# Kernel tuning notes

Hardware: AMD Instinct MI355X
Metric: run time of the kernel (lower is better)

Reference implementation:

```python
import jax, jax.numpy as jnp
import numpy as np
from jax import lax

B, S, H = 32, 512, 128
NEG_INF = -1e30  # matches util.masked_softmax's large negative fill


def setup_inputs() -> dict:
    key = jax.random.key(0)
    ks = jax.random.split(key, 10)
    sc = 0.05
    vp = jax.random.normal(ks[0], (B, S, 2 * H), dtype=jnp.float32)
    # valid lengths in [S//2, S]; packed loop runs max(lengths) steps
    p_s_lengths = jax.random.randint(ks[1], (B,), S // 2, S + 1, dtype=jnp.int32)
    W_vP  = jax.random.normal(ks[2], (H, 2 * H), dtype=jnp.float32) * sc      # linear_vP.weight
    W_vPt = jax.random.normal(ks[3], (H, 2 * H), dtype=jnp.float32) * sc      # linear_vPt.weight
    w_vT  = jax.random.normal(ks[4], (H,), dtype=jnp.float32) * sc            # linear_vT.weight (1,H) -> vector
    W_g   = jax.random.normal(ks[5], (4 * H, 4 * H), dtype=jnp.float32) * sc  # g.weight
    W_ih  = jax.random.normal(ks[6], (3 * H, 4 * H), dtype=jnp.float32) * sc  # GRUCell.weight_ih
    W_hh  = jax.random.normal(ks[7], (3 * H, H), dtype=jnp.float32) * sc      # GRUCell.weight_hh
    b_ih  = jax.random.normal(ks[8], (3 * H,), dtype=jnp.float32) * sc
    b_hh  = jax.random.normal(ks[9], (3 * H,), dtype=jnp.float32) * sc
    return dict(vp=vp, p_s_lengths=p_s_lengths, W_vP=W_vP, W_vPt=W_vPt,
                w_vT=w_vT, W_g=W_g, W_ih=W_ih, W_hh=W_hh, b_ih=b_ih, b_hh=b_hh)


def _self_attn_rnn(vp, p_s_lengths, W_vP, W_vPt, w_vT, W_g, W_ih, W_hh, b_ih, b_hh):
    Bb, Ss, H2 = vp.shape
    Hh = H2 // 2
    s_idx = jnp.arange(Ss)

    # reverse_enc: reverse each sequence only over its valid prefix
    rev_idx = jnp.where(s_idx[None, :] < p_s_lengths[:, None],
                        p_s_lengths[:, None] - 1 - s_idx[None, :], s_idx[None, :])
    rev_vp = jnp.take_along_axis(vp, rev_idx[:, :, None], axis=1)

    bidir_vp = jnp.concatenate([vp, rev_vp], axis=0)       # (2B,S,2H) inputs per step
    vp2 = jnp.concatenate([vp, vp], axis=0)                 # (2B,S,2H) attention memory (forward order!)
    len2 = jnp.concatenate([p_s_lengths, p_s_lengths], 0)   # (2B,)

    keyp = jnp.einsum('bsd,hd->bsh', vp2, W_vP)             # precompute linear_vP(vp)
    seq_mask = s_idx[None, :] < len2[:, None]               # (2B,S)

    def step(h, inputs):
        x_t, active = inputs                                # (2B,2H), (2B,)
        q = x_t @ W_vPt.T                                   # (2B,H)
        logits = jnp.tanh(keyp + q[:, None, :]) @ w_vT      # (2B,S)
        a = jax.nn.softmax(jnp.where(seq_mask, logits, NEG_INF), axis=1)
        ct = jnp.einsum('bs,bsd->bd', a, vp2)               # (2B,2H)
        vpc = jnp.concatenate([x_t, ct], axis=-1)           # (2B,4H)
        gt = jax.nn.sigmoid(vpc @ W_g.T)
        xin = gt * vpc
        gi = xin @ W_ih.T + b_ih
        gh = h @ W_hh.T + b_hh
        ir, iz, inn = jnp.split(gi, 3, axis=-1)
        hr, hz, hn = jnp.split(gh, 3, axis=-1)
        r = jax.nn.sigmoid(ir + hr)
        z = jax.nn.sigmoid(iz + hz)
        n = jnp.tanh(inn + r * hn)
        h_new = (1.0 - z) * n + z * h
        # packed semantics: inactive (padded) slots keep zeros and never update again
        h_new = jnp.where(active[:, None], h_new, 0.0)
        return h_new, h_new

    xs = (jnp.swapaxes(bidir_vp, 0, 1), seq_mask.T)          # (S,2B,2H), (S,2B)
    h0 = jnp.zeros((2 * Bb, Hh), dtype=vp.dtype)
    _, hs = lax.scan(jax.checkpoint(step), h0, xs)           # hs: (S,2B,H)
    hp = jnp.swapaxes(hs, 0, 1)                              # (2B,S,H)
    # original concatenates fwd half and rev half on feature dim (rev half stays in reversed time order)
    return jnp.concatenate([hp[:Bb], hp[Bb:]], axis=-1)      # (B,S,2H)


def reference(vp, p_s_lengths, W_vP, W_vPt, w_vT, W_g, W_ih, W_hh, b_ih, b_hh):
    # dropout is identity at inference (training=False)
    return _self_attn_rnn(vp, p_s_lengths, W_vP, W_vPt, w_vT, W_g, W_ih, W_hh, b_ih, b_hh)
```

## Files before the change

kernel.cpp:

```cpp
#include <hip/hip_runtime.h>
#include <hip/hip_fp16.h>

#define BB 32
#define SS 512
#define HH 128
#define D2 256
#define D3 384
#define D4 512

#define OFF_TK  0
#define OFF_TQ  (OFF_TK + BB*SS*HH)
#define OFF_CT  (OFF_TQ + BB*SS*HH)
#define OFF_GI  (OFF_CT + BB*SS*D2)
#define OFF_F16 (OFF_GI + BB*SS*D3)
#define F16_WG  0
#define F16_WIH (F16_WG + D4*D4)
#define F16_W2  (F16_WIH + D3*D4)

typedef _Float16 f16x8 __attribute__((ext_vector_type(8)));
typedef _Float16 f16x4 __attribute__((ext_vector_type(4)));
typedef float    f32x4 __attribute__((ext_vector_type(4)));
typedef _Float16 h2_t  __attribute__((ext_vector_type(2)));

__device__ __forceinline__ float fast_tanh(float x) {
  float ax = fabsf(x);
  float e  = __expf(-2.0f * ax);
  float t  = __fdividef(1.0f - e, 1.0f + e);
  return x < 0.0f ? -t : t;
}
__device__ __forceinline__ float sigm(float x) {
  return __fdividef(1.0f, 1.0f + __expf(-x));
}

__global__ __launch_bounds__(256) void k0_prep(
    const float* __restrict__ Wg, const float* __restrict__ Wih,
    const float* __restrict__ Wvp, const float* __restrict__ Wvpt,
    float* __restrict__ ws) {
  int i = blockIdx.x * 256 + threadIdx.x;
  _Float16* f16b = (_Float16*)(ws + OFF_F16);
  if (i < D4 * D4) {
    f16b[F16_WG + i] = (_Float16)Wg[i];
  } else if (i < D4 * D4 + D3 * D4) {
    int j = i - D4 * D4;
    f16b[F16_WIH + j] = (_Float16)Wih[j];
  } else {
    int j = i - D4 * D4 - D3 * D4;
    f16b[F16_W2 + j] = (_Float16)(j < HH * D2 ? Wvp[j] : Wvpt[j - HH * D2]);
  }
}

__global__ __launch_bounds__(256, 2) void k1_keyq(const float* __restrict__ vp,
                                                  float* __restrict__ ws) {
  __shared__ __align__(16) _Float16 vpH[64 * 256];
  int tid = threadIdx.x;
  int rows0 = blockIdx.x * 64;

  #pragma unroll
  for (int i = 0; i < 8; ++i) {
    int u = tid + i * 256;
    int r = u >> 5, c8 = u & 31;
    const float* src = vp + (size_t)(rows0 + r) * D2 + c8 * 8;
    float4 a = *(const float4*)src;
    float4 b = *(const float4*)(src + 4);
    f16x8 h;
    h[0]=(_Float16)a.x; h[1]=(_Float16)a.y; h[2]=(_Float16)a.z; h[3]=(_Float16)a.w;
    h[4]=(_Float16)b.x; h[5]=(_Float16)b.y; h[6]=(_Float16)b.z; h[7]=(_Float16)b.w;
    *(f16x8*)(&vpH[r * 256 + (c8 ^ (r & 7)) * 8]) = h;
  }
  __syncthreads();

  const _Float16* W2 = (const _Float16*)(ws + OFF_F16) + F16_W2;
  int w = tid >> 6, l = tid & 63;
  int lr = l & 15, lk = (l >> 4) * 8;

  f32x4 acc[4][4];
  #pragma unroll
  for (int m = 0; m < 4; ++m)
    #pragma unroll
    for (int n = 0; n < 4; ++n) acc[m][n] = (f32x4){0.f, 0.f, 0.f, 0.f};

  for (int kc = 0; kc < 8; ++kc) {
    int k = kc * 32 + lk;
    f16x8 bf[4];
    #pragma unroll
    for (int n = 0; n < 4; ++n) {
      int r = n * 16 + lr;
      bf[n] = *(const f16x8*)(&vpH[r * 256 + (((k >> 3) ^ (r & 7))) * 8]);
    }
    #pragma unroll
    for (int m = 0; m < 4; ++m) {
      int c = w * 64 + m * 16 + lr;
      f16x8 af = *(const f16x8*)(W2 + (size_t)c * 256 + k);
      #pragma unroll
      for (int n = 0; n < 4; ++n)
        acc[m][n] = __builtin_amdgcn_mfma_f32_16x16x32_f16(af, bf[n], acc[m][n], 0, 0, 0);
    }
  }

  int b = rows0 >> 9;
  int s0 = rows0 & 511;
  float* ekT = ws + OFF_TK + (size_t)b * HH * SS;
  float* eqp = ws + OFF_TQ + (size_t)b * SS * HH;
  #pragma unroll
  for (int m = 0; m < 4; ++m) {
    int c0 = w * 64 + m * 16 + (l >> 4) * 4;
    #pragma unroll
    for (int n = 0; n < 4; ++n) {
      int s = s0 + n * 16 + lr;
      float v[4];
      #pragma unroll
      for (int j = 0; j < 4; ++j) {
        float z = fminf(fmaxf(2.0f * acc[m][n][j], -60.0f), 60.0f);
        v[j] = __expf(z);
      }
      if (c0 < HH) {
        #pragma unroll
        for (int j = 0; j < 4; ++j)
          ekT[(size_t)(c0 + j) * SS + s] = v[j];
      } else {
        float4 o; o.x = v[0]; o.y = v[1]; o.z = v[2]; o.w = v[3];
        *(float4*)(eqp + (size_t)s * HH + (c0 - HH)) = o;
      }
    }
  }
}

__global__ __launch_bounds__(256) void k2_attn(const float* __restrict__ vp,
                                               const int* __restrict__ lens,
                                               const float* __restrict__ wvt,
                                               float* __restrict__ ws) {
  int bid = blockIdx.x;
  int b  = (bid & 7) * 4 + ((bid >> 3) & 3);
  int t0 = (bid >> 5) * 16;
  int len = lens[b];
  if (t0 >= len) return;
  int nt = min(16, len - t0);

  __shared__ float L[16][SS];
  __shared__ float Eqs[16][HH];
  __shared__ float inv_sum[16];

  int tid = threadIdx.x;
  const float* EkT = ws + OFF_TK + (size_t)b * HH * SS;
  const float* Eq  = ws + OFF_TQ + (size_t)b * SS * HH;

  for (int idx = tid; idx < 16 * HH; idx += 256) {
    int i = idx >> 7, h = idx & 127;
    Eqs[i][h] = Eq[(size_t)(t0 + i) * HH + h];
  }
  __syncthreads();

  for (int sc = 0; sc < 2; ++sc) {
    int s = tid + sc * 256;
    if (s < len) {
      float acc[16] = {};
      for (int h4 = 0; h4 < 32; ++h4) {
        float k0 = EkT[(size_t)(h4 * 4 + 0) * SS + s];
        float k1 = EkT[(size_t)(h4 * 4 + 1) * SS + s];
        float k2v = EkT[(size_t)(h4 * 4 + 2) * SS + s];
        float k3 = EkT[(size_t)(h4 * 4 + 3) * SS + s];
        const float4 w4 = *(const float4*)(wvt + h4 * 4);
        #pragma unroll
        for (int t = 0; t < 16; ++t) {
          const float4 q4 = *(const float4*)(&Eqs[t][h4 * 4]);
          float r0 = __builtin_amdgcn_rcpf(fmaf(k0, q4.x, 1.0f));
          float r1 = __builtin_amdgcn_rcpf(fmaf(k1, q4.y, 1.0f));
          float r2 = __builtin_amdgcn_rcpf(fmaf(k2v, q4.z, 1.0f));
          float r3 = __builtin_amdgcn_rcpf(fmaf(k3, q4.w, 1.0f));
          float a = acc[t];
          a = fmaf(w4.x, r0, a);
          a = fmaf(w4.y, r1, a);
          a = fmaf(w4.z, r2, a);
          a = fmaf(w4.w, r3, a);
          acc[t] = a;
        }
      }
      #pragma unroll
      for (int t = 0; t < 16; ++t) L[t][s] = -2.0f * acc[t];
    }
  }
  __syncthreads();

  {
    int w = tid >> 6, lane = tid & 63;
    for (int ii = 0; ii < 4; ++ii) {
      int i = w + ii * 4;
      if (i < nt) {
        float m = -1e30f;
        for (int s = lane; s < len; s += 64) m = fmaxf(m, L[i][s]);
        #pragma unroll
        for (int off = 32; off > 0; off >>= 1) m = fmaxf(m, __shfl_xor(m, off));
        float sm = 0.0f;
        for (int s = lane; s < len; s += 64) {
          float e = __expf(L[i][s] - m);
          L[i][s] = e;
          sm += e;
        }
        #pragma unroll
        for (int off = 32; off > 0; off >>= 1) sm += __shfl_xor(sm, off);
        if (lane == 0) inv_sum[i] = __fdividef(1.0f, sm);
      }
    }
  }
  __syncthreads();

  int d4 = (tid & 63) * 4;
  int tg = tid >> 6;
  float4 acc4[4] = {};
  const float* vpb = vp + (size_t)b * SS * D2;
  int s = 0;
  for (; s + 4 <= len; s += 4) {
    #pragma unroll
    for (int u = 0; u < 4; ++u) {
      float4 v4 = *(const float4*)(vpb + (size_t)(s + u) * D2 + d4);
      #pragma unroll
      for (int j = 0; j < 4; ++j) {
        float p = L[tg * 4 + j][s + u];
        acc4[j].x = fmaf(p, v4.x, acc4[j].x);
        acc4[j].y = fmaf(p, v4.y, acc4[j].y);
        acc4[j].z = fmaf(p, v4.z, acc4[j].z);
        acc4[j].w = fmaf(p, v4.w, acc4[j].w);
      }
    }
  }
  for (; s < len; ++s) {
    float4 v4 = *(const float4*)(vpb + (size_t)s * D2 + d4);
    #pragma unroll
    for (int j = 0; j < 4; ++j) {
      float p = L[tg * 4 + j][s];
      acc4[j].x = fmaf(p, v4.x, acc4[j].x);
      acc4[j].y = fmaf(p, v4.y, acc4[j].y);
      acc4[j].z = fmaf(p, v4.z, acc4[j].z);
      acc4[j].w = fmaf(p, v4.w, acc4[j].w);
    }
  }
  float* ctg = ws + OFF_CT + ((size_t)b * SS + t0) * D2;
  #pragma unroll
  for (int j = 0; j < 4; ++j) {
    int t = tg * 4 + j;
    if (t < nt) {
      float is = inv_sum[t];
      float4 o;
      o.x = acc4[j].x * is; o.y = acc4[j].y * is;
      o.z = acc4[j].z * is; o.w = acc4[j].w * is;
      *(float4*)(ctg + (size_t)t * D2 + d4) = o;
    }
  }
}

__global__ __launch_bounds__(256, 2) void k3_gates(const float* __restrict__ vp,
                                                   const int* __restrict__ lens,
                                                   const float* __restrict__ bih,
                                                   float* __restrict__ ws) {
  int b = blockIdx.y;
  int len = lens[b];
  int t0 = blockIdx.x * 32;
  if (t0 >= len) return;

  __shared__ __align__(16) _Float16 vpcH[32 * 512];
  int tid = threadIdx.x;
  const float* ct = ws + OFF_CT;

  #pragma unroll
  for (int i = 0; i < 8; ++i) {
    int u = tid + i * 256;
    int r = u >> 6, c8 = u & 63;
    int c = c8 * 8;
    const float* src = (c < D2) ? (vp + ((size_t)b * SS + t0 + r) * D2 + c)
                                : (ct + ((size_t)b * SS + t0 + r) * D2 + (c - D2));
    float4 a = *(const float4*)src;
    float4 bb = *(const float4*)(src + 4);
    f16x8 h;
    h[0]=(_Float16)a.x;  h[1]=(_Float16)a.y;  h[2]=(_Float16)a.z;  h[3]=(_Float16)a.w;
    h[4]=(_Float16)bb.x; h[5]=(_Float16)bb.y; h[6]=(_Float16)bb.z; h[7]=(_Float16)bb.w;
    *(f16x8*)(&vpcH[r * 512 + (c8 ^ (r & 7)) * 8]) = h;
  }
  __syncthreads();

  const _Float16* WgH  = (const _Float16*)(ws + OFF_F16) + F16_WG;
  const _Float16* WihH = (const _Float16*)(ws + OFF_F16) + F16_WIH;
  int w = tid >> 6, l = tid & 63;
  int lr = l & 15, lk = (l >> 4) * 8;

  f32x4 acc[8][2];
  #pragma unroll
  for (int m = 0; m < 8; ++m) { acc[m][0] = (f32x4){0.f,0.f,0.f,0.f}; acc[m][1] = (f32x4){0.f,0.f,0.f,0.f}; }

  for (int kc = 0; kc < 16; ++kc) {
    int k = kc * 32 + lk;
    f16x8 bf[2];
    #pragma unroll
    for (int n = 0; n < 2; ++n) {
      int r = n * 16 + lr;
      bf[n] = *(const f16x8*)(&vpcH[r * 512 + (((k >> 3) ^ (r & 7))) * 8]);
    }
    #pragma unroll
    for (int m = 0; m < 8; ++m) {
      int c = w * 128 + m * 16 + lr;
      f16x8 af = *(const f16x8*)(WgH + (size_t)c * 512 + k);
      acc[m][0] = __builtin_amdgcn_mfma_f32_16x16x32_f16(af, bf[0], acc[m][0], 0, 0, 0);
      acc[m][1] = __builtin_amdgcn_mfma_f32_16x16x32_f16(af, bf[1], acc[m][1], 0, 0, 0);
    }
  }

  f16x4 xq[8][2];
  #pragma unroll
  for (int m = 0; m < 8; ++m) {
    int c0 = w * 128 + m * 16 + (l >> 4) * 4;
    #pragma unroll
    for (int n = 0; n < 2; ++n) {
      int r = n * 16 + lr;
      int ea = r * 512 + (((c0 >> 3) ^ (r & 7))) * 8 + (c0 & 7);
      f16x4 vq = *(const f16x4*)(&vpcH[ea]);
      f16x4 xo;
      #pragma unroll
      for (int j = 0; j < 4; ++j)
        xo[j] = (_Float16)(sigm(acc[m][n][j]) * (float)vq[j]);
      xq[m][n] = xo;
    }
  }
  __syncthreads();
  #pragma unroll
  for (int m = 0; m < 8; ++m) {
    int c0 = w * 128 + m * 16 + (l >> 4) * 4;
    #pragma unroll
    for (int n = 0; n < 2; ++n) {
      int r = n * 16 + lr;
      int ea = r * 512 + (((c0 >> 3) ^ (r & 7))) * 8 + (c0 & 7);
      *(f16x4*)(&vpcH[ea]) = xq[m][n];
    }
  }
  __syncthreads();

  f32x4 gacc[6][2];
  #pragma unroll
  for (int m = 0; m < 6; ++m) { gacc[m][0] = (f32x4){0.f,0.f,0.f,0.f}; gacc[m][1] = (f32x4){0.f,0.f,0.f,0.f}; }

  for (int kc = 0; kc < 16; ++kc) {
    int k = kc * 32 + lk;
    f16x8 bf[2];
    #pragma unroll
    for (int n = 0; n < 2; ++n) {
      int r = n * 16 + lr;
      bf[n] = *(const f16x8*)(&vpcH[r * 512 + (((k >> 3) ^ (r & 7))) * 8]);
    }
    #pragma unroll
    for (int m = 0; m < 6; ++m) {
      int c = w * 96 + m * 16 + lr;
      f16x8 af = *(const f16x8*)(WihH + (size_t)c * 512 + k);
      gacc[m][0] = __builtin_amdgcn_mfma_f32_16x16x32_f16(af, bf[0], gacc[m][0], 0, 0, 0);
      gacc[m][1] = __builtin_amdgcn_mfma_f32_16x16x32_f16(af, bf[1], gacc[m][1], 0, 0, 0);
    }
  }

  float* gig = ws + OFF_GI;
  #pragma unroll
  for (int m = 0; m < 6; ++m) {
    int c0 = w * 96 + m * 16 + (l >> 4) * 4;
    float4 bq = *(const float4*)(bih + c0);
    #pragma unroll
    for (int n = 0; n < 2; ++n) {
      int r = n * 16 + lr;
      float4 o;
      o.x = gacc[m][n][0] + bq.x;
      o.y = gacc[m][n][1] + bq.y;
      o.z = gacc[m][n][2] + bq.z;
      o.w = gacc[m][n][3] + bq.w;
      *(float4*)(gig + ((size_t)b * SS + t0 + r) * D3 + c0) = o;
    }
  }
}

__global__ __launch_bounds__(128, 1) void k4_scan(const float* __restrict__ whh,
                                                  const float* __restrict__ bhh,
                                                  const int* __restrict__ lens,
                                                  const float* __restrict__ ws,
                                                  float* __restrict__ out) {
  int bid = blockIdx.x;
  int xcd = bid & 7, dir = (bid >> 3) & 1, q = bid >> 4;
  int b = xcd * 4 + q;
  int len = lens[b];
  int tid = threadIdx.x;
  const float* gi = ws + OFF_GI + (size_t)b * SS * D3;

  h2_t w0[64], w1[64], w2[64];
  {
    const float* r0 = whh + (size_t)tid * HH;
    const float* r1 = whh + (size_t)(tid + 128) * HH;
    const float* r2 = whh + (size_t)(tid + 256) * HH;
    #pragma unroll
    for (int k = 0; k < 64; ++k) {
      w0[k] = h2_t{(_Float16)r0[2 * k], (_Float16)r0[2 * k + 1]};
      w1[k] = h2_t{(_Float16)r1[2 * k], (_Float16)r1[2 * k + 1]};
      w2[k] = h2_t{(_Float16)r2[2 * k], (_Float16)r2[2 * k + 1]};
    }
  }
  float bh0 = bhh[tid], bh1 = bhh[tid + 128], bh2 = bhh[tid + 256];

  __shared__ __align__(16) _Float16 hbuf[2][128];
  hbuf[0][tid] = (_Float16)0.0f;
  float h_own = 0.0f;

  float* outb = out + (size_t)b * SS * D2 + dir * HH;

#define K4_BAR() do {                                                          \
    asm volatile("s_waitcnt lgkmcnt(0)" ::: "memory");                         \
    __builtin_amdgcn_s_barrier();                                              \
    __builtin_amdgcn_sched_barrier(0);                                         \
  } while (0)

#define K4_PF(gx0, gx1, gx2, tnext) do {                                       \
    int tp = (tnext) < len ? (tnext) : (len - 1);                              \
    int tgp = dir ? (len - 1 - tp) : tp;                                       \
    const float* gp = gi + (size_t)tgp * D3;                                   \
    gx0 = gp[tid]; gx1 = gp[tid + 128]; gx2 = gp[tid + 256];                   \
  } while (0)

#define K4_STEP(gx0, gx1, gx2, tstep, PB) do {                                 \
    const f16x8* hb8 = (const f16x8*)hbuf[PB];                                 \
    float a00 = 0.f, a01 = 0.f, a02 = 0.f, a03 = 0.f;                          \
    float a10 = 0.f, a11 = 0.f, a12 = 0.f, a13 = 0.f;                          \
    float a20 = 0.f, a21 = 0.f, a22 = 0.f, a23 = 0.f;                          \
    _Pragma("unroll")                                                          \
    for (int k8 = 0; k8 < 16; ++k8) {                                          \
      f16x8 hv = hb8[k8];                                                      \
      h2_t p0 = __builtin_shufflevector(hv, hv, 0, 1);                         \
      h2_t p1 = __builtin_shufflevector(hv, hv, 2, 3);                         \
      h2_t p2 = __builtin_shufflevector(hv, hv, 4, 5);                         \
      h2_t p3 = __builtin_shufflevector(hv, hv, 6, 7);                         \
      a00 = __builtin_amdgcn_fdot2(p0, w0[4 * k8 + 0], a00, false);            \
      a01 = __builtin_amdgcn_fdot2(p1, w0[4 * k8 + 1], a01, false);            \
      a02 = __builtin_amdgcn_fdot2(p2, w0[4 * k8 + 2], a02, false);            \
      a03 = __builtin_amdgcn_fdot2(p3, w0[4 * k8 + 3], a03, false);            \
      a10 = __builtin_amdgcn_fdot2(p0, w1[4 * k8 + 0], a10, false);            \
      a11 = __builtin_amdgcn_fdot2(p1, w1[4 * k8 + 1], a11, false);            \
      a12 = __builtin_amdgcn_fdot2(p2, w1[4 * k8 + 2], a12, false);            \
      a13 = __builtin_amdgcn_fdot2(p3, w1[4 * k8 + 3], a13, false);            \
      a20 = __builtin_amdgcn_fdot2(p0, w2[4 * k8 + 0], a20, false);            \
      a21 = __builtin_amdgcn_fdot2(p1, w2[4 * k8 + 1], a21, false);            \
      a22 = __builtin_amdgcn_fdot2(p2, w2[4 * k8 + 2], a22, false);            \
      a23 = __builtin_amdgcn_fdot2(p3, w2[4 * k8 + 3], a23, false);            \
    }                                                                          \
    float gh0 = ((a00 + a01) + (a02 + a03)) + bh0;                             \
    float gh1 = ((a10 + a11) + (a12 + a13)) + bh1;                             \
    float gh2 = ((a20 + a21) + (a22 + a23)) + bh2;                             \
    float r = sigm((gx0) + gh0);                                               \
    float z = sigm((gx1) + gh1);                                               \
    float n = fast_tanh(fmaf(r, gh2, (gx2)));                                  \
    float hn = (1.0f - z) * n + z * h_own;                                     \
    h_own = hn;                                                                \
    outb[(size_t)(tstep) * D2 + tid] = hn;                                     \
    hbuf[(PB) ^ 1][tid] = (_Float16)hn;                                        \
    K4_PF(gx0, gx1, gx2, (tstep) + 4);                                         \
    K4_BAR();                                                                  \
  } while (0)

  float gA0, gA1, gA2, gB0, gB1, gB2, gC0, gC1, gC2, gD0, gD1, gD2;
  K4_PF(gA0, gA1, gA2, 0);
  K4_PF(gB0, gB1, gB2, 1);
  K4_PF(gC0, gC1, gC2, 2);
  K4_PF(gD0, gD1, gD2, 3);
  K4_BAR();

  int t = 0;
  while (t + 3 < len) {
    K4_STEP(gA0, gA1, gA2, t,     0);
    K4_STEP(gB0, gB1, gB2, t + 1, 1);
    K4_STEP(gC0, gC1, gC2, t + 2, 0);
    K4_STEP(gD0, gD1, gD2, t + 3, 1);
    t += 4;
  }
  if (t < len)     K4_STEP(gA0, gA1, gA2, t,     0);
  if (t + 1 < len) K4_STEP(gB0, gB1, gB2, t + 1, 1);
  if (t + 2 < len) K4_STEP(gC0, gC1, gC2, t + 2, 0);

#undef K4_STEP
#undef K4_PF
#undef K4_BAR
}

extern "C" void kernel_launch(void* const* d_in, const int* in_sizes, int n_in,
                              void* d_out, int out_size, void* d_ws, size_t ws_size,
                              hipStream_t stream) {
  const float* vp   = (const float*)d_in[0];
  const int*   lens = (const int*)d_in[1];
  const float* Wvp  = (const float*)d_in[2];
  const float* Wvpt = (const float*)d_in[3];
  const float* wvt  = (const float*)d_in[4];
  const float* Wg   = (const float*)d_in[5];
  const float* Wih  = (const float*)d_in[6];
  const float* Whh  = (const float*)d_in[7];
  const float* bih  = (const float*)d_in[8];
  const float* bhh  = (const float*)d_in[9];
  float* out = (float*)d_out;
  float* ws  = (float*)d_ws;

  hipMemsetAsync(d_out, 0, (size_t)out_size * sizeof(float), stream);

  k0_prep<<<2048, 256, 0, stream>>>(Wg, Wih, Wvp, Wvpt, ws);
  k1_keyq<<<BB * SS / 64, 256, 0, stream>>>(vp, ws);
  k2_attn<<<1024, 256, 0, stream>>>(vp, lens, wvt, ws);
  k3_gates<<<dim3(SS / 32, BB), 256, 0, stream>>>(vp, lens, bih, ws);
  k4_scan<<<64, 128, 0, stream>>>(Whh, bhh, lens, ws, out);
}
```

Baseline: 606.3 us.

## Split GRU scan hidden-dot across two half-waves with shuffle reduction

The recurrent scan kernel now uses 256 threads per block instead of 128. Each hidden unit's W_hh dot product is split across two lanes, each covering half of the K dimension, and the partial sums are combined with a cross-half-wave xor shuffle. This halves the serial fdot2 chain per step and the per-thread register-resident weights. The costs are idle lanes during the gate math, an extra shuffle per gate, and a barrier that now spans four waves.

```diff
diff --git a/kernel.cpp b/kernel.cpp
--- a/kernel.cpp
+++ b/kernel.cpp
@@ -371,7 +371,7 @@
   }
 }
 
-__global__ __launch_bounds__(128, 1) void k4_scan(const float* __restrict__ whh,
+__global__ __launch_bounds__(256, 1) void k4_scan(const float* __restrict__ whh,
                                                   const float* __restrict__ bhh,
                                                   const int* __restrict__ lens,
                                                   const float* __restrict__ ws,
@@ -381,24 +381,27 @@
   int b = xcd * 4 + q;
   int len = lens[b];
   int tid = threadIdx.x;
+  int wv = tid >> 6, l = tid & 63;
+  int j = wv * 32 + (l & 31);
+  int p = l >> 5;
   const float* gi = ws + OFF_GI + (size_t)b * SS * D3;
 
-  h2_t w0[64], w1[64], w2[64];
+  h2_t w0[32], w1[32], w2[32];
   {
-    const float* r0 = whh + (size_t)tid * HH;
-    const float* r1 = whh + (size_t)(tid + 128) * HH;
-    const float* r2 = whh + (size_t)(tid + 256) * HH;
-    #pragma unroll
-    for (int k = 0; k < 64; ++k) {
+    const float* r0 = whh + (size_t)j * HH + p * 64;
+    const float* r1 = whh + (size_t)(j + 128) * HH + p * 64;
+    const float* r2 = whh + (size_t)(j + 256) * HH + p * 64;
+    #pragma unroll
+    for (int k = 0; k < 32; ++k) {
       w0[k] = h2_t{(_Float16)r0[2 * k], (_Float16)r0[2 * k + 1]};
       w1[k] = h2_t{(_Float16)r1[2 * k], (_Float16)r1[2 * k + 1]};
       w2[k] = h2_t{(_Float16)r2[2 * k], (_Float16)r2[2 * k + 1]};
     }
   }
-  float bh0 = bhh[tid], bh1 = bhh[tid + 128], bh2 = bhh[tid + 256];
+  float bh0 = bhh[j], bh1 = bhh[j + 128], bh2 = bhh[j + 256];
 
   __shared__ __align__(16) _Float16 hbuf[2][128];
-  hbuf[0][tid] = (_Float16)0.0f;
+  if (tid < 128) hbuf[0][tid] = (_Float16)0.0f;
   float h_own = 0.0f;
 
   float* outb = out + (size_t)b * SS * D2 + dir * HH;
@@ -410,52 +413,62 @@
   } while (0)
 
 #define K4_PF(gx0, gx1, gx2, tnext) do {                                       \
-    int tp = (tnext) < len ? (tnext) : (len - 1);                              \
-    int tgp = dir ? (len - 1 - tp) : tp;                                       \
-    const float* gp = gi + (size_t)tgp * D3;                                   \
-    gx0 = gp[tid]; gx1 = gp[tid + 128]; gx2 = gp[tid + 256];                   \
+    if (p == 0) {                                                              \
+      int tp = (tnext) < len ? (tnext) : (len - 1);                            \
+      int tgp = dir ? (len - 1 - tp) : tp;                                     \
+      const float* gp = gi + (size_t)tgp * D3;                                 \
+      gx0 = gp[j]; gx1 = gp[j + 128]; gx2 = gp[j + 256];                       \
+    }                                                                          \
   } while (0)
 
 #define K4_STEP(gx0, gx1, gx2, tstep, PB) do {                                 \
-    const f16x8* hb8 = (const f16x8*)hbuf[PB];                                 \
+    const f16x8* hb8 = (const f16x8*)&hbuf[PB][p * 64];                        \
     float a00 = 0.f, a01 = 0.f, a02 = 0.f, a03 = 0.f;                          \
     float a10 = 0.f, a11 = 0.f, a12 = 0.f, a13 = 0.f;                          \
     float a20 = 0.f, a21 = 0.f, a22 = 0.f, a23 = 0.f;                          \
     _Pragma("unroll")                                                          \
-    for (int k8 = 0; k8 < 16; ++k8) {                                          \
+    for (int k8 = 0; k8 < 8; ++k8) {                                           \
       f16x8 hv = hb8[k8];                                                      \
-      h2_t p0 = __builtin_shufflevector(hv, hv, 0, 1);                         \
-      h2_t p1 = __builtin_shufflevector(hv, hv, 2, 3);                         \
-      h2_t p2 = __builtin_shufflevector(hv, hv, 4, 5);                         \
-      h2_t p3 = __builtin_shufflevector(hv, hv, 6, 7);                         \
-      a00 = __builtin_amdgcn_fdot2(p0, w0[4 * k8 + 0], a00, false);            \
-      a01 = __builtin_amdgcn_fdot2(p1, w0[4 * k8 + 1], a01, false);            \
-      a02 = __builtin_amdgcn_fdot2(p2, w0[4 * k8 + 2], a02, false);            \
-      a03 = __builtin_amdgcn_fdot2(p3, w0[4 * k8 + 3], a03, false);            \
-      a10 = __builtin_amdgcn_fdot2(p0, w1[4 * k8 + 0], a10, false);            \
-      a11 = __builtin_amdgcn_fdot2(p1, w1[4 * k8 + 1], a11, false);            \
-      a12 = __builtin_amdgcn_fdot2(p2, w1[4 * k8 + 2], a12, false);            \
-      a13 = __builtin_amdgcn_fdot2(p3, w1[4 * k8 + 3], a13, false);            \
-      a20 = __builtin_amdgcn_fdot2(p0, w2[4 * k8 + 0], a20, false);            \
-      a21 = __builtin_amdgcn_fdot2(p1, w2[4 * k8 + 1], a21, false);            \
-      a22 = __builtin_amdgcn_fdot2(p2, w2[4 * k8 + 2], a22, false);            \
-      a23 = __builtin_amdgcn_fdot2(p3, w2[4 * k8 + 3], a23, false);            \
+      h2_t q0 = __builtin_shufflevector(hv, hv, 0, 1);                         \
+      h2_t q1 = __builtin_shufflevector(hv, hv, 2, 3);                         \
+      h2_t q2 = __builtin_shufflevector(hv, hv, 4, 5);                         \
+      h2_t q3 = __builtin_shufflevector(hv, hv, 6, 7);                         \
+      a00 = __builtin_amdgcn_fdot2(q0, w0[4 * k8 + 0], a00, false);            \
+      a01 = __builtin_amdgcn_fdot2(q1, w0[4 * k8 + 1], a01, false);            \
+      a02 = __builtin_amdgcn_fdot2(q2, w0[4 * k8 + 2], a02, false);            \
+      a03 = __builtin_amdgcn_fdot2(q3, w0[4 * k8 + 3], a03, false);            \
+      a10 = __builtin_amdgcn_fdot2(q0, w1[4 * k8 + 0], a10, false);            \
+      a11 = __builtin_amdgcn_fdot2(q1, w1[4 * k8 + 1], a11, false);            \
+      a12 = __builtin_amdgcn_fdot2(q2, w1[4 * k8 + 2], a12, false);            \
+      a13 = __builtin_amdgcn_fdot2(q3, w1[4 * k8 + 3], a13, false);            \
+      a20 = __builtin_amdgcn_fdot2(q0, w2[4 * k8 + 0], a20, false);            \
+      a21 = __builtin_amdgcn_fdot2(q1, w2[4 * k8 + 1], a21, false);            \
+      a22 = __builtin_amdgcn_fdot2(q2, w2[4 * k8 + 2], a22, false);            \
+      a23 = __builtin_amdgcn_fdot2(q3, w2[4 * k8 + 3], a23, false);            \
     }                                                                          \
-    float gh0 = ((a00 + a01) + (a02 + a03)) + bh0;                             \
-    float gh1 = ((a10 + a11) + (a12 + a13)) + bh1;                             \
-    float gh2 = ((a20 + a21) + (a22 + a23)) + bh2;                             \
-    float r = sigm((gx0) + gh0);                                               \
-    float z = sigm((gx1) + gh1);                                               \
-    float n = fast_tanh(fmaf(r, gh2, (gx2)));                                  \
-    float hn = (1.0f - z) * n + z * h_own;                                     \
-    h_own = hn;                                                                \
-    outb[(size_t)(tstep) * D2 + tid] = hn;                                     \
-    hbuf[(PB) ^ 1][tid] = (_Float16)hn;                                        \
+    float s0 = ((a00 + a01) + (a02 + a03));                                    \
+    float s1 = ((a10 + a11) + (a12 + a13));                                    \
+    float s2 = ((a20 + a21) + (a22 + a23));                                    \
+    s0 += __shfl_xor(s0, 32);                                                  \
+    s1 += __shfl_xor(s1, 32);                                                  \
+    s2 += __shfl_xor(s2, 32);                                                  \
+    if (p == 0) {                                                              \
+      float r = sigm((gx0) + s0 + bh0);                                        \
+      float z = sigm((gx1) + s1 + bh1);                                        \
+      float n = fast_tanh(fmaf(r, s2 + bh2, (gx2)));                           \
+      float hn = (1.0f - z) * n + z * h_own;                                   \
+      h_own = hn;                                                              \
+      outb[(size_t)(tstep) * D2 + j] = hn;                                     \
+      hbuf[(PB) ^ 1][j] = (_Float16)hn;                                        \
+    }                                                                          \
     K4_PF(gx0, gx1, gx2, (tstep) + 4);                                         \
     K4_BAR();                                                                  \
   } while (0)
 
-  float gA0, gA1, gA2, gB0, gB1, gB2, gC0, gC1, gC2, gD0, gD1, gD2;
+  float gA0 = 0.f, gA1 = 0.f, gA2 = 0.f;
+  float gB0 = 0.f, gB1 = 0.f, gB2 = 0.f;
+  float gC0 = 0.f, gC1 = 0.f, gC2 = 0.f;
+  float gD0 = 0.f, gD1 = 0.f, gD2 = 0.f;
   K4_PF(gA0, gA1, gA2, 0);
   K4_PF(gB0, gB1, gB2, 1);
   K4_PF(gC0, gC1, gC2, 2);
@@ -501,5 +514,5 @@
   k1_keyq<<<BB * SS / 64, 256, 0, stream>>>(vp, ws);
   k2_attn<<<1024, 256, 0, stream>>>(vp, lens, wvt, ws);
   k3_gates<<<dim3(SS / 32, BB), 256, 0, stream>>>(vp, lens, bih, ws);
-  k4_scan<<<64, 128, 0, stream>>>(Whh, bhh, lens, ws, out);
-}
+  k4_scan<<<64, 256, 0, stream>>>(Whh, bhh, lens, ws, out);
+}
```

Result: faster. 530.8 us (-12.5%).

## Batch 16 GRU sequences per block and compute recurrence with MFMA

Applied to the files above, without the earlier changes.

The GRU scan kernel changes from one 128-thread block per (batch, direction) that uses fdot2 with weights held in registers to 4 blocks of 512 threads. Each block packs 8 batches times 2 directions as the N=16 dimension of MFMA 16x16x32 f16 ops, with W_hh fragments held in registers and hidden states in an XOR-swizzled LDS buffer. The block runs max(len) steps over its group and masks inactive sequences. This cuts per-step instruction count by using matrix cores, but it uses only 4 CUs and forces each group to run as long as its longest sequence.

```diff
diff --git a/kernel.cpp b/kernel.cpp
--- a/kernel.cpp
+++ b/kernel.cpp
@@ -371,37 +371,52 @@
   }
 }
 
-__global__ __launch_bounds__(128, 1) void k4_scan(const float* __restrict__ whh,
+__global__ __launch_bounds__(512, 1) void k4_scan(const float* __restrict__ whh,
                                                   const float* __restrict__ bhh,
                                                   const int* __restrict__ lens,
                                                   const float* __restrict__ ws,
                                                   float* __restrict__ out) {
-  int bid = blockIdx.x;
-  int xcd = bid & 7, dir = (bid >> 3) & 1, q = bid >> 4;
-  int b = xcd * 4 + q;
+  int blk = blockIdx.x;
+  int tid = threadIdx.x;
+  int w = tid >> 6, l = tid & 63;
+  int seq = l & 15;
+  int b_local = seq & 7, dir = seq >> 3;
+  int b = blk * 8 + b_local;
   int len = lens[b];
-  int tid = threadIdx.x;
-  const float* gi = ws + OFF_GI + (size_t)b * SS * D3;
-
-  h2_t w0[64], w1[64], w2[64];
-  {
-    const float* r0 = whh + (size_t)tid * HH;
-    const float* r1 = whh + (size_t)(tid + 128) * HH;
-    const float* r2 = whh + (size_t)(tid + 256) * HH;
-    #pragma unroll
-    for (int k = 0; k < 64; ++k) {
-      w0[k] = h2_t{(_Float16)r0[2 * k], (_Float16)r0[2 * k + 1]};
-      w1[k] = h2_t{(_Float16)r1[2 * k], (_Float16)r1[2 * k + 1]};
-      w2[k] = h2_t{(_Float16)r2[2 * k], (_Float16)r2[2 * k + 1]};
-    }
-  }
-  float bh0 = bhh[tid], bh1 = bhh[tid + 128], bh2 = bhh[tid + 256];
-
-  __shared__ __align__(16) _Float16 hbuf[2][128];
-  hbuf[0][tid] = (_Float16)0.0f;
-  float h_own = 0.0f;
-
-  float* outb = out + (size_t)b * SS * D2 + dir * HH;
+  int maxlen = 0;
+  #pragma unroll
+  for (int i = 0; i < 8; ++i) {
+    int li = lens[blk * 8 + i];
+    maxlen = li > maxlen ? li : maxlen;
+  }
+
+  int j0 = 16 * w + ((l >> 4) << 2);
+
+  f16x8 afr[3][4];
+  #pragma unroll
+  for (int g = 0; g < 3; ++g) {
+    int row = 128 * g + 16 * w + (l & 15);
+    #pragma unroll
+    for (int kc = 0; kc < 4; ++kc) {
+      const float* ap = whh + (size_t)row * HH + kc * 32 + (l >> 4) * 8;
+      float4 x = *(const float4*)ap;
+      float4 y = *(const float4*)(ap + 4);
+      f16x8 f;
+      f[0]=(_Float16)x.x; f[1]=(_Float16)x.y; f[2]=(_Float16)x.z; f[3]=(_Float16)x.w;
+      f[4]=(_Float16)y.x; f[5]=(_Float16)y.y; f[6]=(_Float16)y.z; f[7]=(_Float16)y.w;
+      afr[g][kc] = f;
+    }
+  }
+  f32x4 bh0 = *(const f32x4*)(bhh + 0 * 128 + j0);
+  f32x4 bh1 = *(const f32x4*)(bhh + 1 * 128 + j0);
+  f32x4 bh2 = *(const f32x4*)(bhh + 2 * 128 + j0);
+
+  __shared__ __align__(16) _Float16 hb[2 * 16 * 128];
+  for (int i = tid; i < 2048; i += 512) hb[i] = (_Float16)0.0f;
+
+  f32x4 h_own = (f32x4){0.f, 0.f, 0.f, 0.f};
+  const float* gi_b = ws + OFF_GI + (size_t)b * SS * D3;
+  float* outp = out + (size_t)b * SS * D2 + dir * HH + j0;
 
 #define K4_BAR() do {                                                          \
     asm volatile("s_waitcnt lgkmcnt(0)" ::: "memory");                         \
@@ -409,53 +424,63 @@
     __builtin_amdgcn_sched_barrier(0);                                         \
   } while (0)
 
-#define K4_PF(gx0, gx1, gx2, tnext) do {                                       \
+#define K4_PF(GV0, GV1, GV2, tnext) do {                                       \
     int tp = (tnext) < len ? (tnext) : (len - 1);                              \
-    int tgp = dir ? (len - 1 - tp) : tp;                                       \
-    const float* gp = gi + (size_t)tgp * D3;                                   \
-    gx0 = gp[tid]; gx1 = gp[tid + 128]; gx2 = gp[tid + 256];                   \
+    int tg = dir ? (len - 1 - tp) : tp;                                        \
+    const float* gp = gi_b + (size_t)tg * D3;                                  \
+    GV0 = *(const f32x4*)(gp + 0 * 128 + j0);                                  \
+    GV1 = *(const f32x4*)(gp + 1 * 128 + j0);                                  \
+    GV2 = *(const f32x4*)(gp + 2 * 128 + j0);                                  \
   } while (0)
 
-#define K4_STEP(gx0, gx1, gx2, tstep, PB) do {                                 \
-    const f16x8* hb8 = (const f16x8*)hbuf[PB];                                 \
-    float a00 = 0.f, a01 = 0.f, a02 = 0.f, a03 = 0.f;                          \
-    float a10 = 0.f, a11 = 0.f, a12 = 0.f, a13 = 0.f;                          \
-    float a20 = 0.f, a21 = 0.f, a22 = 0.f, a23 = 0.f;                          \
+#define K4_STEP(GV0, GV1, GV2, tstep, PB) do {                                 \
+    const _Float16* hbR = hb + (PB) * 2048;                                    \
+    f16x8 bf0, bf1, bf2, bf3;                                                  \
+    {                                                                          \
+      int kb = (l >> 4) * 8;                                                   \
+      int sw = (seq & 7) << 3;                                                 \
+      bf0 = *(const f16x8*)(hbR + seq * 128 + ((kb +  0) ^ sw));               \
+      bf1 = *(const f16x8*)(hbR + seq * 128 + ((kb + 32) ^ sw));               \
+      bf2 = *(const f16x8*)(hbR + seq * 128 + ((kb + 64) ^ sw));               \
+      bf3 = *(const f16x8*)(hbR + seq * 128 + ((kb + 96) ^ sw));               \
+    }                                                                          \
+    f32x4 ac0 = (f32x4){0.f,0.f,0.f,0.f};                                      \
+    f32x4 ac1 = (f32x4){0.f,0.f,0.f,0.f};                                      \
+    f32x4 ac2 = (f32x4){0.f,0.f,0.f,0.f};                                      \
+    ac0 = __builtin_amdgcn_mfma_f32_16x16x32_f16(afr[0][0], bf0, ac0, 0,0,0);  \
+    ac1 = __builtin_amdgcn_mfma_f32_16x16x32_f16(afr[1][0], bf0, ac1, 0,0,0);  \
+    ac2 = __builtin_amdgcn_mfma_f32_16x16x32_f16(afr[2][0], bf0, ac2, 0,0,0);  \
+    ac0 = __builtin_amdgcn_mfma_f32_16x16x32_f16(afr[0][1], bf1, ac0, 0,0,0);  \
+    ac1 = __builtin_amdgcn_mfma_f32_16x16x32_f16(afr[1][1], bf1, ac1, 0,0,0);  \
+    ac2 = __builtin_amdgcn_mfma_f32_16x16x32_f16(afr[2][1], bf1, ac2, 0,0,0);  \
+    ac0 = __builtin_amdgcn_mfma_f32_16x16x32_f16(afr[0][2], bf2, ac0, 0,0,0);  \
+    ac1 = __builtin_amdgcn_mfma_f32_16x16x32_f16(afr[1][2], bf2, ac1, 0,0,0);  \
+    ac2 = __builtin_amdgcn_mfma_f32_16x16x32_f16(afr[2][2], bf2, ac2, 0,0,0);  \
+    ac0 = __builtin_amdgcn_mfma_f32_16x16x32_f16(afr[0][3], bf3, ac0, 0,0,0);  \
+    ac1 = __builtin_amdgcn_mfma_f32_16x16x32_f16(afr[1][3], bf3, ac1, 0,0,0);  \
+    ac2 = __builtin_amdgcn_mfma_f32_16x16x32_f16(afr[2][3], bf3, ac2, 0,0,0);  \
+    bool active = (tstep) < len;                                               \
+    f16x4 hq;                                                                  \
     _Pragma("unroll")                                                          \
-    for (int k8 = 0; k8 < 16; ++k8) {                                          \
-      f16x8 hv = hb8[k8];                                                      \
-      h2_t p0 = __builtin_shufflevector(hv, hv, 0, 1);                         \
-      h2_t p1 = __builtin_shufflevector(hv, hv, 2, 3);                         \
-      h2_t p2 = __builtin_shufflevector(hv, hv, 4, 5);                         \
-      h2_t p3 = __builtin_shufflevector(hv, hv, 6, 7);                         \
-      a00 = __builtin_amdgcn_fdot2(p0, w0[4 * k8 + 0], a00, false);            \
-      a01 = __builtin_amdgcn_fdot2(p1, w0[4 * k8 + 1], a01, false);            \
-      a02 = __builtin_amdgcn_fdot2(p2, w0[4 * k8 + 2], a02, false);            \
-      a03 = __builtin_amdgcn_fdot2(p3, w0[4 * k8 + 3], a03, false);            \
-      a10 = __builtin_amdgcn_fdot2(p0, w1[4 * k8 + 0], a10, false);            \
-      a11 = __builtin_amdgcn_fdot2(p1, w1[4 * k8 + 1], a11, false);            \
-      a12 = __builtin_amdgcn_fdot2(p2, w1[4 * k8 + 2], a12, false);            \
-      a13 = __builtin_amdgcn_fdot2(p3, w1[4 * k8 + 3], a13, false);            \
-      a20 = __builtin_amdgcn_fdot2(p0, w2[4 * k8 + 0], a20, false);            \
-      a21 = __builtin_amdgcn_fdot2(p1, w2[4 * k8 + 1], a21, false);            \
-      a22 = __builtin_amdgcn_fdot2(p2, w2[4 * k8 + 2], a22, false);            \
-      a23 = __builtin_amdgcn_fdot2(p3, w2[4 * k8 + 3], a23, false);            \
+    for (int i = 0; i < 4; ++i) {                                              \
+      float rr = sigm(GV0[i] + ac0[i] + bh0[i]);                               \
+      float zz = sigm(GV1[i] + ac1[i] + bh1[i]);                               \
+      float nn = fast_tanh(fmaf(rr, ac2[i] + bh2[i], GV2[i]));                 \
+      float hn = (1.0f - zz) * nn + zz * h_own[i];                             \
+      hn = active ? hn : 0.0f;                                                 \
+      h_own[i] = hn;                                                           \
+      hq[i] = (_Float16)hn;                                                    \
     }                                                                          \
-    float gh0 = ((a00 + a01) + (a02 + a03)) + bh0;                             \
-    float gh1 = ((a10 + a11) + (a12 + a13)) + bh1;                             \
-    float gh2 = ((a20 + a21) + (a22 + a23)) + bh2;                             \
-    float r = sigm((gx0) + gh0);                                               \
-    float z = sigm((gx1) + gh1);                                               \
-    float n = fast_tanh(fmaf(r, gh2, (gx2)));                                  \
-    float hn = (1.0f - z) * n + z * h_own;                                     \
-    h_own = hn;                                                                \
-    outb[(size_t)(tstep) * D2 + tid] = hn;                                     \
-    hbuf[(PB) ^ 1][tid] = (_Float16)hn;                                        \
-    K4_PF(gx0, gx1, gx2, (tstep) + 4);                                         \
+    if (active) *(f32x4*)(outp + (size_t)(tstep) * D2) = h_own;                \
+    {                                                                          \
+      _Float16* hbW = hb + ((PB) ^ 1) * 2048;                                  \
+      *(f16x4*)(hbW + seq * 128 + (j0 ^ ((seq & 7) << 3))) = hq;               \
+    }                                                                          \
+    K4_PF(GV0, GV1, GV2, (tstep) + 4);                                         \
     K4_BAR();                                                                  \
   } while (0)
 
-  float gA0, gA1, gA2, gB0, gB1, gB2, gC0, gC1, gC2, gD0, gD1, gD2;
+  f32x4 gA0, gA1, gA2, gB0, gB1, gB2, gC0, gC1, gC2, gD0, gD1, gD2;
   K4_PF(gA0, gA1, gA2, 0);
   K4_PF(gB0, gB1, gB2, 1);
   K4_PF(gC0, gC1, gC2, 2);
@@ -463,16 +488,16 @@
   K4_BAR();
 
   int t = 0;
-  while (t + 3 < len) {
+  while (t + 3 < maxlen) {
     K4_STEP(gA0, gA1, gA2, t,     0);
     K4_STEP(gB0, gB1, gB2, t + 1, 1);
     K4_STEP(gC0, gC1, gC2, t + 2, 0);
     K4_STEP(gD0, gD1, gD2, t + 3, 1);
     t += 4;
   }
-  if (t < len)     K4_STEP(gA0, gA1, gA2, t,     0);
-  if (t + 1 < len) K4_STEP(gB0, gB1, gB2, t + 1, 1);
-  if (t + 2 < len) K4_STEP(gC0, gC1, gC2, t + 2, 0);
+  if (t < maxlen)     K4_STEP(gA0, gA1, gA2, t,     0);
+  if (t + 1 < maxlen) K4_STEP(gB0, gB1, gB2, t + 1, 1);
+  if (t + 2 < maxlen) K4_STEP(gC0, gC1, gC2, t + 2, 0);
 
 #undef K4_STEP
 #undef K4_PF
@@ -501,5 +526,5 @@
   k1_keyq<<<BB * SS / 64, 256, 0, stream>>>(vp, ws);
   k2_attn<<<1024, 256, 0, stream>>>(vp, lens, wvt, ws);
   k3_gates<<<dim3(SS / 32, BB), 256, 0, stream>>>(vp, lens, bih, ws);
-  k4_scan<<<64, 128, 0, stream>>>(Whh, bhh, lens, ws, out);
-}
+  k4_scan<<<4, 512, 0, stream>>>(Whh, bhh, lens, ws, out);
+}
```

New measurement: 786.5 us. +29.7%, slower.
